# Optimization experiments

Measured on AMD Instinct MI355X. Metric: run time of the kernel, lower is better.

## Reference

```python
import jax, jax.numpy as jnp
import numpy as np


def _bilinear_sample(img, gx, gy):
    # img: [B,C,H,W]; gx,gy: [B,N] normalized coords in [-1,1]
    # Matches torch F.grid_sample(mode='bilinear', padding_mode='border', align_corners=False)
    B, C, H, W = img.shape
    ix = ((gx + 1.0) * W - 1.0) * 0.5
    iy = ((gy + 1.0) * H - 1.0) * 0.5
    ix = jnp.clip(ix, 0.0, W - 1.0)  # border padding: clip source coords
    iy = jnp.clip(iy, 0.0, H - 1.0)
    x0 = jnp.floor(ix); y0 = jnp.floor(iy)
    wx = ix - x0; wy = iy - y0
    x0i = x0.astype(jnp.int32); y0i = y0.astype(jnp.int32)
    x1i = jnp.minimum(x0i + 1, W - 1); y1i = jnp.minimum(y0i + 1, H - 1)
    imt = jnp.transpose(img, (0, 2, 3, 1))  # [B,H,W,C]
    b = jnp.arange(B)[:, None]
    v00 = imt[b, y0i, x0i]  # [B,N,C]
    v01 = imt[b, y0i, x1i]
    v10 = imt[b, y1i, x0i]
    v11 = imt[b, y1i, x1i]
    w00 = ((1 - wy) * (1 - wx))[..., None]
    w01 = ((1 - wy) * wx)[..., None]
    w10 = (wy * (1 - wx))[..., None]
    w11 = (wy * wx)[..., None]
    out = v00 * w00 + v01 * w01 + v10 * w10 + v11 * w11  # [B,N,C]
    return jnp.transpose(out, (0, 2, 1))  # [B,C,N]


def _conv1x1(W, b, x):
    # W: [Cout,Cin], b: [Cout], x: [B,Cin,N] -> [B,Cout,N]
    return jnp.einsum('oc,bcn->bon', W, x) + b[None, :, None]


def setup_inputs() -> dict:
    key = jax.random.key(0)
    ks = jax.random.split(key, 12)
    B, N = 4, 65536
    C_FEAT = 64
    CH = [67, 128, 128]
    x_loc = jax.random.uniform(ks[0], (B, 3, N), dtype=jnp.float32)
    x_feat = jax.random.normal(ks[1], (B, C_FEAT, N), dtype=jnp.float32)
    m0 = jax.random.normal(ks[2], (B, 64, 128, 128), dtype=jnp.float32)
    m1 = jax.random.normal(ks[3], (B, 128, 128, 128), dtype=jnp.float32)
    m2 = jax.random.normal(ks[4], (B, 256, 128, 128), dtype=jnp.float32)
    # SharedMLP params (kaiming-ish scale)
    W1 = jax.random.normal(ks[5], (CH[1], CH[0]), dtype=jnp.float32) * (1.0 / np.sqrt(CH[0]))
    b1 = jnp.zeros((CH[1],), dtype=jnp.float32)
    W2 = jax.random.normal(ks[6], (CH[2], CH[1]), dtype=jnp.float32) * (1.0 / np.sqrt(CH[1]))
    b2 = jnp.zeros((CH[2],), dtype=jnp.float32)
    # resid_loc: zero-init except identity on first two input channels (x/y of x_loc)
    Wr = jnp.zeros((2, CH[2] + 3), dtype=jnp.float32).at[0, 0].set(1.0).at[1, 1].set(1.0)
    br = jnp.zeros((2,), dtype=jnp.float32)
    return dict(x_loc=x_loc, x_feat=x_feat, m0=m0, m1=m1, m2=m2,
                W1=W1, b1=b1, W2=W2, b2=b2, Wr=Wr, br=br)


def reference(x_loc, x_feat, m0, m1, m2, W1, b1, W2, b2, Wr, br):
    # loc = Sequential(SharedMLP([67,128,128]), ReLU)
    h = jnp.concatenate([x_loc, x_feat], axis=1)          # [B,67,N]
    h = jax.nn.relu(_conv1x1(W1, b1, h))                  # [B,128,N]
    h = jax.nn.relu(_conv1x1(W2, b2, h))                  # [B,128,N]
    h = jnp.concatenate([x_loc, h], axis=1)               # [B,131,N]
    grid = _conv1x1(Wr, br, h)                            # [B,2,N]
    gx, gy = grid[:, 0, :], grid[:, 1, :]                 # grid last dim = (x, y)
    pooled = [_bilinear_sample(m, gx, gy) for m in (m0, m1, m2)]
    return jnp.concatenate(pooled, axis=1)                # [B,448,N]
```

## Files before the change

### kernel.cpp

```cpp
#include <hip/hip_runtime.h>
#include <hip/hip_bf16.h>

typedef __bf16 bf16x8 __attribute__((ext_vector_type(8)));
typedef __bf16 bf16x4 __attribute__((ext_vector_type(4)));
typedef float  f32x4  __attribute__((ext_vector_type(4)));

#define N_PTS  65536
#define B_SZ   4
#define P_TOT  (B_SZ * N_PTS)
#define PITCH1 104
#define PITCH2 136

__device__ __forceinline__ void gload_lds16(const float* g, float* l) {
    __builtin_amdgcn_global_load_lds(
        (const __attribute__((address_space(1))) void*)g,
        (__attribute__((address_space(3))) void*)l,
        16, 0, 0);
}

__global__ __launch_bounds__(256) void mlp_grid_kernel(
    const float* __restrict__ x_loc, const float* __restrict__ x_feat,
    const float* __restrict__ W1, const float* __restrict__ b1,
    const float* __restrict__ W2, const float* __restrict__ b2,
    const float* __restrict__ Wr, const float* __restrict__ br,
    float* __restrict__ grid_out)
{
    __shared__ __align__(16) union SmemU {
        __bf16 wbuf[128 * 128];
        struct {
            __bf16 stage[64 * PITCH1];
            __bf16 h1s[64 * PITCH2];
            float  gpart[16][2][64];
        } r;
    } u;

    const int tid = threadIdx.x;
    const int w   = tid >> 6;
    const int l   = tid & 63;
    const int q   = l >> 4;
    const int lp  = l & 15;

    for (int idx = tid; idx < 128 * 96; idx += 256) {
        const int o = idx / 96;
        const int k = idx - o * 96;
        u.wbuf[idx] = (__bf16)((k < 67) ? W1[o * 67 + k] : 0.0f);
    }
    __syncthreads();
    bf16x8 w1f[2][3];
    #pragma unroll
    for (int i = 0; i < 2; ++i) {
        const int o = (2 * w + i) * 16 + lp;
        #pragma unroll
        for (int ks = 0; ks < 3; ++ks)
            w1f[i][ks] = *(const bf16x8*)&u.wbuf[o * 96 + ks * 32 + q * 8];
    }
    __syncthreads();
    for (int idx = tid; idx < 128 * 128; idx += 256)
        u.wbuf[idx] = (__bf16)W2[idx];
    __syncthreads();
    bf16x8 w2f[2][4];
    #pragma unroll
    for (int i = 0; i < 2; ++i) {
        const int o = (2 * w + i) * 16 + lp;
        #pragma unroll
        for (int ks = 0; ks < 4; ++ks)
            w2f[i][ks] = *(const bf16x8*)&u.wbuf[o * 128 + ks * 32 + q * 8];
    }
    float b1v[2][4], b2v[2][4], wrp[2][2][4];
    #pragma unroll
    for (int i = 0; i < 2; ++i) {
        const int ob = (2 * w + i) * 16 + q * 4;
        #pragma unroll
        for (int r = 0; r < 4; ++r) {
            b1v[i][r]    = b1[ob + r];
            b2v[i][r]    = b2[ob + r];
            wrp[0][i][r] = Wr[0 * 131 + 3 + ob + r];
            wrp[1][i][r] = Wr[1 * 131 + 3 + ob + r];
        }
    }
    __syncthreads();

    for (int t = 0; t < 4; ++t) {
        const int pt0 = blockIdx.x * 256 + t * 64;

        {
            const int g4  = tid & 15;
            const int kk  = tid >> 4;
            const int ptg = g4 * 4;
            const int pp  = pt0 + ptg;
            const int bb  = pp >> 16;
            const int nn  = pp & 0xFFFF;
            for (int k = kk; k < 96; k += 16) {
                if (k < 67) {
                    const float4 v = (k < 3)
                        ? *(const float4*)&x_loc[((bb * 3 + k) << 16) | nn]
                        : *(const float4*)&x_feat[((bb * 64 + (k - 3)) << 16) | nn];
                    u.r.stage[(ptg + 0) * PITCH1 + k] = (__bf16)v.x;
                    u.r.stage[(ptg + 1) * PITCH1 + k] = (__bf16)v.y;
                    u.r.stage[(ptg + 2) * PITCH1 + k] = (__bf16)v.z;
                    u.r.stage[(ptg + 3) * PITCH1 + k] = (__bf16)v.w;
                } else if (k >= 67) {
                    u.r.stage[(ptg + 0) * PITCH1 + k] = (__bf16)0.0f;
                    u.r.stage[(ptg + 1) * PITCH1 + k] = (__bf16)0.0f;
                    u.r.stage[(ptg + 2) * PITCH1 + k] = (__bf16)0.0f;
                    u.r.stage[(ptg + 3) * PITCH1 + k] = (__bf16)0.0f;
                }
            }
        }
        __syncthreads();

        for (int col = 0; col < 4; ++col) {
            const int pt = col * 16 + lp;
            bf16x8 bfr[3];
            #pragma unroll
            for (int ks = 0; ks < 3; ++ks)
                bfr[ks] = *(const bf16x8*)&u.r.stage[pt * PITCH1 + ks * 32 + q * 8];
            #pragma unroll
            for (int i = 0; i < 2; ++i) {
                f32x4 acc = {0.f, 0.f, 0.f, 0.f};
                #pragma unroll
                for (int ks = 0; ks < 3; ++ks)
                    acc = __builtin_amdgcn_mfma_f32_16x16x32_bf16(w1f[i][ks], bfr[ks], acc, 0, 0, 0);
                bf16x4 hv;
                #pragma unroll
                for (int r = 0; r < 4; ++r)
                    hv[r] = (__bf16)fmaxf(acc[r] + b1v[i][r], 0.0f);
                *(bf16x4*)&u.r.h1s[pt * PITCH2 + (2 * w + i) * 16 + q * 4] = hv;
            }
        }
        __syncthreads();

        for (int col = 0; col < 4; ++col) {
            const int pt = col * 16 + lp;
            bf16x8 bfr[4];
            #pragma unroll
            for (int ks = 0; ks < 4; ++ks)
                bfr[ks] = *(const bf16x8*)&u.r.h1s[pt * PITCH2 + ks * 32 + q * 8];
            float p0 = 0.f, p1 = 0.f;
            #pragma unroll
            for (int i = 0; i < 2; ++i) {
                f32x4 acc = {0.f, 0.f, 0.f, 0.f};
                #pragma unroll
                for (int ks = 0; ks < 4; ++ks)
                    acc = __builtin_amdgcn_mfma_f32_16x16x32_bf16(w2f[i][ks], bfr[ks], acc, 0, 0, 0);
                #pragma unroll
                for (int r = 0; r < 4; ++r) {
                    const float v = fmaxf(acc[r] + b2v[i][r], 0.0f);
                    p0 += wrp[0][i][r] * v;
                    p1 += wrp[1][i][r] * v;
                }
            }
            u.r.gpart[w * 4 + q][0][pt] = p0;
            u.r.gpart[w * 4 + q][1][pt] = p1;
        }
        __syncthreads();

        if (tid < 128) {
            const int o  = tid >> 6;
            const int pt = tid & 63;
            const int pp = pt0 + pt;
            const int bb = pp >> 16;
            const int nn = pp & 0xFFFF;
            float s = br[o];
            #pragma unroll
            for (int c = 0; c < 3; ++c)
                s += Wr[o * 131 + c] * x_loc[((bb * 3 + c) << 16) | nn];
            #pragma unroll
            for (int g = 0; g < 16; ++g) s += u.r.gpart[g][o][pt];
            grid_out[o * P_TOT + pp] = s;
        }
    }
}

__global__ __launch_bounds__(1024) void sample_kernel(
    const float* __restrict__ m0, const float* __restrict__ m1,
    const float* __restrict__ m2, const float* __restrict__ grid,
    float* __restrict__ out)
{
    __shared__ float sbuf[2][128 * 128];
    __shared__ int redmn[16], redmx[16];

    const int tid  = threadIdx.x;
    const int wv   = tid >> 6;
    const int lane = tid & 63;
    const int p = blockIdx.x * 1024 + tid;
    const int b = p >> 16;
    const int n = p & 0xFFFF;
    const float gx = grid[p];
    const float gy = grid[P_TOT + p];

    float ix = ((gx + 1.0f) * 128.0f - 1.0f) * 0.5f;
    float iy = ((gy + 1.0f) * 128.0f - 1.0f) * 0.5f;
    ix = fminf(fmaxf(ix, 0.0f), 127.0f);
    iy = fminf(fmaxf(iy, 0.0f), 127.0f);
    const float x0f = floorf(ix);
    const float y0f = floorf(iy);
    const float wx = ix - x0f;
    const float wy = iy - y0f;
    const int x0 = (int)x0f, y0 = (int)y0f;
    const int x1 = min(x0 + 1, 127);
    const int y1 = min(y0 + 1, 127);
    const float w00 = (1.f - wy) * (1.f - wx);
    const float w01 = (1.f - wy) * wx;
    const float w10 = wy * (1.f - wx);
    const float w11 = wy * wx;

    int mn = y0, mx = y1;
    #pragma unroll
    for (int s = 32; s; s >>= 1) {
        mn = min(mn, __shfl_xor(mn, s));
        mx = max(mx, __shfl_xor(mx, s));
    }
    if (lane == 0) { redmn[wv] = mn; redmx[wv] = mx; }
    __syncthreads();
    #pragma unroll
    for (int i = 0; i < 16; ++i) { mn = min(mn, redmn[i]); mx = max(mx, redmx[i]); }

    int ymin = mn;
    int R = mx - mn + 1;
    if (R & 1) { if (ymin > 0) --ymin; ++R; }
    const int nchunk = R >> 1;

    const int a00 = (y0 - ymin) * 128 + x0;
    const int d01 = x1 - x0;
    const int d10 = (y1 - y0) * 128;

    auto slice = [&](int c) -> const float* {
        if (c < 64)  return m0 + ((size_t)(b * 64  + c)         << 14);
        if (c < 192) return m1 + ((size_t)(b * 128 + (c - 64))  << 14);
        return              m2 + ((size_t)(b * 256 + (c - 192)) << 14);
    };
    auto stage = [&](const float* src, int bsel) {
        const float* g = src + ymin * 128 + (lane << 2);
        for (int ch = wv; ch < nchunk; ch += 16)
            gload_lds16(g + (ch << 8), &sbuf[bsel][ch << 8]);
    };

    float* op = out + (size_t)(b * 448) * 65536 + n;

    stage(slice(0), 0);
    for (int c = 0; c < 448; ++c) {
        const int cur = c & 1;
        __syncthreads();
        if (c + 1 < 448) stage(slice(c + 1), cur ^ 1);
        const float* sb = sbuf[cur];
        const float v00 = sb[a00];
        const float v01 = sb[a00 + d01];
        const float v10 = sb[a00 + d10];
        const float v11 = sb[a00 + d01 + d10];
        const float v = w00 * v00 + w01 * v01 + w10 * v10 + w11 * v11;
        __builtin_nontemporal_store(v, op);
        op += 65536;
    }
}

extern "C" void kernel_launch(void* const* d_in, const int* in_sizes, int n_in,
                              void* d_out, int out_size, void* d_ws, size_t ws_size,
                              hipStream_t stream)
{
    (void)in_sizes; (void)n_in; (void)out_size; (void)ws_size;
    const float* x_loc  = (const float*)d_in[0];
    const float* x_feat = (const float*)d_in[1];
    const float* m0     = (const float*)d_in[2];
    const float* m1     = (const float*)d_in[3];
    const float* m2     = (const float*)d_in[4];
    const float* W1     = (const float*)d_in[5];
    const float* b1     = (const float*)d_in[6];
    const float* W2     = (const float*)d_in[7];
    const float* b2     = (const float*)d_in[8];
    const float* Wr     = (const float*)d_in[9];
    const float* br     = (const float*)d_in[10];
    float* out  = (float*)d_out;
    float* grid = (float*)d_ws;

    mlp_grid_kernel<<<dim3(P_TOT / 256), dim3(256), 0, stream>>>(
        x_loc, x_feat, W1, b1, W2, b2, Wr, br, grid);
    sample_kernel<<<dim3(P_TOT / 1024), dim3(1024), 0, stream>>>(
        m0, m1, m2, grid, out);
}
```

Before: 1.131 ms.

## Fuse MLP grid computation into sampler with bounding-box LDS staging

Merges the MLP grid kernel and the bilinear sampler into one 512-thread kernel that keeps grid coordinates in LDS instead of a workspace round-trip. Weights are pre-packed into MFMA fragment layout by a small one-block kernel. The sampler now stages only the x/y bounding box of each block's sample footprint (72-wide padded rows) with triple buffering and deferred stores, falling back to direct global gathers when the box is too large. This cuts LDS traffic per channel and raises occupancy, at the cost of an extra launch and a slow fallback path for scattered grids.

```diff
diff --git a/kernel.cpp b/kernel.cpp
--- a/kernel.cpp
+++ b/kernel.cpp
@@ -10,6 +10,11 @@
 #define P_TOT  (B_SZ * N_PTS)
 #define PITCH1 104
 #define PITCH2 136
+#define CPAD   72
+#define BUF_F  6144
+#define NCH    448
+#define WP1_ELEMS (8*3*64*8)
+#define WP2_ELEMS (8*4*64*8)
 
 __device__ __forceinline__ void gload_lds16(const float* g, float* l) {
     __builtin_amdgcn_global_load_lds(
@@ -18,92 +23,105 @@
         16, 0, 0);
 }
 
-__global__ __launch_bounds__(256) void mlp_grid_kernel(
+__global__ __launch_bounds__(256) void repack_weights(
+    const float* __restrict__ W1, const float* __restrict__ W2,
+    __bf16* __restrict__ wp)
+{
+    const int tid = threadIdx.x;
+    for (int idx = tid; idx < WP1_ELEMS; idx += 256) {
+        const int j8   = idx & 7;
+        const int l    = (idx >> 3) & 63;
+        const int rest = idx >> 9;
+        const int ks   = rest % 3;
+        const int j    = rest / 3;
+        const int row  = j * 16 + (l & 15);
+        const int k    = ks * 32 + ((l >> 4) << 3) + j8;
+        wp[idx] = (__bf16)((k < 67) ? W1[row * 67 + k] : 0.0f);
+    }
+    for (int idx = tid; idx < WP2_ELEMS; idx += 256) {
+        const int j8   = idx & 7;
+        const int l    = (idx >> 3) & 63;
+        const int rest = idx >> 9;
+        const int ks   = rest & 3;
+        const int j    = rest >> 2;
+        const int row  = j * 16 + (l & 15);
+        const int k    = ks * 32 + ((l >> 4) << 3) + j8;
+        wp[WP1_ELEMS + idx] = (__bf16)W2[row * 128 + k];
+    }
+}
+
+__global__ __launch_bounds__(512, 4) void fused_kernel(
     const float* __restrict__ x_loc, const float* __restrict__ x_feat,
-    const float* __restrict__ W1, const float* __restrict__ b1,
-    const float* __restrict__ W2, const float* __restrict__ b2,
+    const float* __restrict__ m0, const float* __restrict__ m1,
+    const float* __restrict__ m2,
+    const __bf16* __restrict__ wp,
+    const float* __restrict__ b1, const float* __restrict__ b2,
     const float* __restrict__ Wr, const float* __restrict__ br,
-    float* __restrict__ grid_out)
+    float* __restrict__ out)
 {
-    __shared__ __align__(16) union SmemU {
-        __bf16 wbuf[128 * 128];
+    __shared__ __align__(16) union Smem {
         struct {
             __bf16 stage[64 * PITCH1];
             __bf16 h1s[64 * PITCH2];
-            float  gpart[16][2][64];
-        } r;
+            float  gpart[8][2][64];
+            float  gxy[2][512];
+        } m;
+        float sbuf[3][BUF_F];
     } u;
+    __shared__ int redY0[8], redY1[8], redX0[8], redX1[8];
 
     const int tid = threadIdx.x;
     const int w   = tid >> 6;
     const int l   = tid & 63;
     const int q   = l >> 4;
     const int lp  = l & 15;
-
-    for (int idx = tid; idx < 128 * 96; idx += 256) {
-        const int o = idx / 96;
-        const int k = idx - o * 96;
-        u.wbuf[idx] = (__bf16)((k < 67) ? W1[o * 67 + k] : 0.0f);
-    }
-    __syncthreads();
-    bf16x8 w1f[2][3];
+    const int blk = blockIdx.x;
+    const int b   = blk >> 7;
+    const int n0  = (blk & 127) << 9;
+
+    bf16x8 w1f[3], w2f[4];
     #pragma unroll
-    for (int i = 0; i < 2; ++i) {
-        const int o = (2 * w + i) * 16 + lp;
-        #pragma unroll
-        for (int ks = 0; ks < 3; ++ks)
-            w1f[i][ks] = *(const bf16x8*)&u.wbuf[o * 96 + ks * 32 + q * 8];
-    }
-    __syncthreads();
-    for (int idx = tid; idx < 128 * 128; idx += 256)
-        u.wbuf[idx] = (__bf16)W2[idx];
-    __syncthreads();
-    bf16x8 w2f[2][4];
+    for (int ks = 0; ks < 3; ++ks)
+        w1f[ks] = *(const bf16x8*)&wp[((w * 3 + ks) * 64 + l) * 8];
     #pragma unroll
-    for (int i = 0; i < 2; ++i) {
-        const int o = (2 * w + i) * 16 + lp;
-        #pragma unroll
-        for (int ks = 0; ks < 4; ++ks)
-            w2f[i][ks] = *(const bf16x8*)&u.wbuf[o * 128 + ks * 32 + q * 8];
-    }
-    float b1v[2][4], b2v[2][4], wrp[2][2][4];
-    #pragma unroll
-    for (int i = 0; i < 2; ++i) {
-        const int ob = (2 * w + i) * 16 + q * 4;
+    for (int ks = 0; ks < 4; ++ks)
+        w2f[ks] = *(const bf16x8*)&wp[WP1_ELEMS + ((w * 4 + ks) * 64 + l) * 8];
+    float b1v[4], b2v[4], wrp0[4], wrp1[4];
+    {
+        const int ob = w * 16 + q * 4;
         #pragma unroll
         for (int r = 0; r < 4; ++r) {
-            b1v[i][r]    = b1[ob + r];
-            b2v[i][r]    = b2[ob + r];
-            wrp[0][i][r] = Wr[0 * 131 + 3 + ob + r];
-            wrp[1][i][r] = Wr[1 * 131 + 3 + ob + r];
-        }
-    }
-    __syncthreads();
-
-    for (int t = 0; t < 4; ++t) {
-        const int pt0 = blockIdx.x * 256 + t * 64;
+            b1v[r]  = b1[ob + r];
+            b2v[r]  = b2[ob + r];
+            wrp0[r] = Wr[0 * 131 + 3 + ob + r];
+            wrp1[r] = Wr[1 * 131 + 3 + ob + r];
+        }
+    }
+
+    for (int t = 0; t < 8; ++t) {
+        const int pt0n = n0 + t * 64;
 
         {
             const int g4  = tid & 15;
             const int kk  = tid >> 4;
             const int ptg = g4 * 4;
-            const int pp  = pt0 + ptg;
-            const int bb  = pp >> 16;
-            const int nn  = pp & 0xFFFF;
-            for (int k = kk; k < 96; k += 16) {
+            const int nn  = pt0n + ptg;
+            #pragma unroll
+            for (int kx = 0; kx < 3; ++kx) {
+                const int k = kk + kx * 32;
                 if (k < 67) {
                     const float4 v = (k < 3)
-                        ? *(const float4*)&x_loc[((bb * 3 + k) << 16) | nn]
-                        : *(const float4*)&x_feat[((bb * 64 + (k - 3)) << 16) | nn];
-                    u.r.stage[(ptg + 0) * PITCH1 + k] = (__bf16)v.x;
-                    u.r.stage[(ptg + 1) * PITCH1 + k] = (__bf16)v.y;
-                    u.r.stage[(ptg + 2) * PITCH1 + k] = (__bf16)v.z;
-                    u.r.stage[(ptg + 3) * PITCH1 + k] = (__bf16)v.w;
-                } else if (k >= 67) {
-                    u.r.stage[(ptg + 0) * PITCH1 + k] = (__bf16)0.0f;
-                    u.r.stage[(ptg + 1) * PITCH1 + k] = (__bf16)0.0f;
-                    u.r.stage[(ptg + 2) * PITCH1 + k] = (__bf16)0.0f;
-                    u.r.stage[(ptg + 3) * PITCH1 + k] = (__bf16)0.0f;
+                        ? *(const float4*)&x_loc[((b * 3 + k) << 16) | nn]
+                        : *(const float4*)&x_feat[((b * 64 + (k - 3)) << 16) | nn];
+                    u.m.stage[(ptg + 0) * PITCH1 + k] = (__bf16)v.x;
+                    u.m.stage[(ptg + 1) * PITCH1 + k] = (__bf16)v.y;
+                    u.m.stage[(ptg + 2) * PITCH1 + k] = (__bf16)v.z;
+                    u.m.stage[(ptg + 3) * PITCH1 + k] = (__bf16)v.w;
+                } else {
+                    u.m.stage[(ptg + 0) * PITCH1 + k] = (__bf16)0.0f;
+                    u.m.stage[(ptg + 1) * PITCH1 + k] = (__bf16)0.0f;
+                    u.m.stage[(ptg + 2) * PITCH1 + k] = (__bf16)0.0f;
+                    u.m.stage[(ptg + 3) * PITCH1 + k] = (__bf16)0.0f;
                 }
             }
         }
@@ -114,19 +132,16 @@
             bf16x8 bfr[3];
             #pragma unroll
             for (int ks = 0; ks < 3; ++ks)
-                bfr[ks] = *(const bf16x8*)&u.r.stage[pt * PITCH1 + ks * 32 + q * 8];
-            #pragma unroll
-            for (int i = 0; i < 2; ++i) {
-                f32x4 acc = {0.f, 0.f, 0.f, 0.f};
-                #pragma unroll
-                for (int ks = 0; ks < 3; ++ks)
-                    acc = __builtin_amdgcn_mfma_f32_16x16x32_bf16(w1f[i][ks], bfr[ks], acc, 0, 0, 0);
-                bf16x4 hv;
-                #pragma unroll
-                for (int r = 0; r < 4; ++r)
-                    hv[r] = (__bf16)fmaxf(acc[r] + b1v[i][r], 0.0f);
-                *(bf16x4*)&u.r.h1s[pt * PITCH2 + (2 * w + i) * 16 + q * 4] = hv;
-            }
+                bfr[ks] = *(const bf16x8*)&u.m.stage[pt * PITCH1 + ks * 32 + q * 8];
+            f32x4 acc = {0.f, 0.f, 0.f, 0.f};
+            #pragma unroll
+            for (int ks = 0; ks < 3; ++ks)
+                acc = __builtin_amdgcn_mfma_f32_16x16x32_bf16(w1f[ks], bfr[ks], acc, 0, 0, 0);
+            bf16x4 hv;
+            #pragma unroll
+            for (int r = 0; r < 4; ++r)
+                hv[r] = (__bf16)fmaxf(acc[r] + b1v[r], 0.0f);
+            *(bf16x4*)&u.m.h1s[pt * PITCH2 + w * 16 + q * 4] = hv;
         }
         __syncthreads();
 
@@ -135,59 +150,45 @@
             bf16x8 bfr[4];
             #pragma unroll
             for (int ks = 0; ks < 4; ++ks)
-                bfr[ks] = *(const bf16x8*)&u.r.h1s[pt * PITCH2 + ks * 32 + q * 8];
+                bfr[ks] = *(const bf16x8*)&u.m.h1s[pt * PITCH2 + ks * 32 + q * 8];
+            f32x4 acc = {0.f, 0.f, 0.f, 0.f};
+            #pragma unroll
+            for (int ks = 0; ks < 4; ++ks)
+                acc = __builtin_amdgcn_mfma_f32_16x16x32_bf16(w2f[ks], bfr[ks], acc, 0, 0, 0);
             float p0 = 0.f, p1 = 0.f;
             #pragma unroll
-            for (int i = 0; i < 2; ++i) {
-                f32x4 acc = {0.f, 0.f, 0.f, 0.f};
-                #pragma unroll
-                for (int ks = 0; ks < 4; ++ks)
-                    acc = __builtin_amdgcn_mfma_f32_16x16x32_bf16(w2f[i][ks], bfr[ks], acc, 0, 0, 0);
-                #pragma unroll
-                for (int r = 0; r < 4; ++r) {
-                    const float v = fmaxf(acc[r] + b2v[i][r], 0.0f);
-                    p0 += wrp[0][i][r] * v;
-                    p1 += wrp[1][i][r] * v;
-                }
+            for (int r = 0; r < 4; ++r) {
+                const float v = fmaxf(acc[r] + b2v[r], 0.0f);
+                p0 += wrp0[r] * v;
+                p1 += wrp1[r] * v;
             }
-            u.r.gpart[w * 4 + q][0][pt] = p0;
-            u.r.gpart[w * 4 + q][1][pt] = p1;
+            p0 += __shfl_xor(p0, 16); p0 += __shfl_xor(p0, 32);
+            p1 += __shfl_xor(p1, 16); p1 += __shfl_xor(p1, 32);
+            if (q == 0) {
+                u.m.gpart[w][0][pt] = p0;
+                u.m.gpart[w][1][pt] = p1;
+            }
         }
         __syncthreads();
 
         if (tid < 128) {
             const int o  = tid >> 6;
             const int pt = tid & 63;
-            const int pp = pt0 + pt;
-            const int bb = pp >> 16;
-            const int nn = pp & 0xFFFF;
+            const int nn = pt0n + pt;
             float s = br[o];
             #pragma unroll
             for (int c = 0; c < 3; ++c)
-                s += Wr[o * 131 + c] * x_loc[((bb * 3 + c) << 16) | nn];
-            #pragma unroll
-            for (int g = 0; g < 16; ++g) s += u.r.gpart[g][o][pt];
-            grid_out[o * P_TOT + pp] = s;
-        }
-    }
-}
-
-__global__ __launch_bounds__(1024) void sample_kernel(
-    const float* __restrict__ m0, const float* __restrict__ m1,
-    const float* __restrict__ m2, const float* __restrict__ grid,
-    float* __restrict__ out)
-{
-    __shared__ float sbuf[2][128 * 128];
-    __shared__ int redmn[16], redmx[16];
-
-    const int tid  = threadIdx.x;
-    const int wv   = tid >> 6;
-    const int lane = tid & 63;
-    const int p = blockIdx.x * 1024 + tid;
-    const int b = p >> 16;
-    const int n = p & 0xFFFF;
-    const float gx = grid[p];
-    const float gy = grid[P_TOT + p];
+                s += Wr[o * 131 + c] * x_loc[((b * 3 + c) << 16) | nn];
+            #pragma unroll
+            for (int g = 0; g < 8; ++g) s += u.m.gpart[g][o][pt];
+            u.m.gxy[o][t * 64 + pt] = s;
+        }
+    }
+    __syncthreads();
+
+    const float gx = u.m.gxy[0][tid];
+    const float gy = u.m.gxy[1][tid];
+    const int n = n0 + tid;
 
     float ix = ((gx + 1.0f) * 128.0f - 1.0f) * 0.5f;
     float iy = ((gy + 1.0f) * 128.0f - 1.0f) * 0.5f;
@@ -205,52 +206,89 @@
     const float w10 = wy * (1.f - wx);
     const float w11 = wy * wx;
 
-    int mn = y0, mx = y1;
+    int mnY = y0, mxY = y1, mnX = x0, mxX = x1;
     #pragma unroll
     for (int s = 32; s; s >>= 1) {
-        mn = min(mn, __shfl_xor(mn, s));
-        mx = max(mx, __shfl_xor(mx, s));
-    }
-    if (lane == 0) { redmn[wv] = mn; redmx[wv] = mx; }
+        mnY = min(mnY, __shfl_xor(mnY, s));
+        mxY = max(mxY, __shfl_xor(mxY, s));
+        mnX = min(mnX, __shfl_xor(mnX, s));
+        mxX = max(mxX, __shfl_xor(mxX, s));
+    }
+    if (l == 0) { redY0[w] = mnY; redY1[w] = mxY; redX0[w] = mnX; redX1[w] = mxX; }
     __syncthreads();
     #pragma unroll
-    for (int i = 0; i < 16; ++i) { mn = min(mn, redmn[i]); mx = max(mx, redmx[i]); }
-
-    int ymin = mn;
-    int R = mx - mn + 1;
-    if (R & 1) { if (ymin > 0) --ymin; ++R; }
-    const int nchunk = R >> 1;
-
-    const int a00 = (y0 - ymin) * 128 + x0;
-    const int d01 = x1 - x0;
-    const int d10 = (y1 - y0) * 128;
-
-    auto slice = [&](int c) -> const float* {
+    for (int i = 0; i < 8; ++i) {
+        mnY = min(mnY, redY0[i]); mxY = max(mxY, redY1[i]);
+        mnX = min(mnX, redX0[i]); mxX = max(mxX, redX1[i]);
+    }
+
+    const int ymin  = mnY;
+    const int R     = mxY - mnY + 1;
+    const int xminA = mnX & ~3;
+    const int width = mxX - xminA + 1;
+    const bool ok   = (width <= CPAD) && (R * CPAD <= BUF_F);
+
+    auto slice_ptr = [&](int c) -> const float* {
         if (c < 64)  return m0 + ((size_t)(b * 64  + c)         << 14);
         if (c < 192) return m1 + ((size_t)(b * 128 + (c - 64))  << 14);
         return              m2 + ((size_t)(b * 256 + (c - 192)) << 14);
     };
-    auto stage = [&](const float* src, int bsel) {
-        const float* g = src + ymin * 128 + (lane << 2);
-        for (int ch = wv; ch < nchunk; ch += 16)
-            gload_lds16(g + (ch << 8), &sbuf[bsel][ch << 8]);
-    };
-
-    float* op = out + (size_t)(b * 448) * 65536 + n;
-
-    stage(slice(0), 0);
-    for (int c = 0; c < 448; ++c) {
-        const int cur = c & 1;
-        __syncthreads();
-        if (c + 1 < 448) stage(slice(c + 1), cur ^ 1);
-        const float* sb = sbuf[cur];
-        const float v00 = sb[a00];
-        const float v01 = sb[a00 + d01];
-        const float v10 = sb[a00 + d10];
-        const float v11 = sb[a00 + d01 + d10];
-        const float v = w00 * v00 + w01 * v01 + w10 * v10 + w11 * v11;
-        __builtin_nontemporal_store(v, op);
-        op += 65536;
+
+    float* op = out + ((size_t)(b * 448) << 16) + n;
+
+    if (ok) {
+        const int nchunk = (R * CPAD + 255) >> 8;
+        const int a00 = (y0 - ymin) * CPAD + (x0 - xminA);
+        const int d01 = x1 - x0;
+        const int d10 = (y1 - y0) * CPAD;
+
+        auto stage = [&](int c, int bsel) {
+            const float* sp   = slice_ptr(c);
+            const float* src  = sp + ymin * 128 + xminA;
+            const float* gend = sp + 16384 - 4;
+            for (int ch = w; ch < nchunk; ch += 8) {
+                const int o   = (ch << 8) + (l << 2);
+                const int row = o / CPAD;
+                const int col = o - row * CPAD;
+                const float* g = src + row * 128 + col;
+                if (g > gend) g = gend;
+                gload_lds16(g, &u.sbuf[bsel][ch << 8]);
+            }
+        };
+
+        stage(0, 0);
+        stage(1, 1);
+        float vprev = 0.f;
+        float* opprev = op;
+        int cur = 0, nst = 2;
+        for (int c = 0; c < NCH; ++c) {
+            __syncthreads();
+            if (c) __builtin_nontemporal_store(vprev, opprev);
+            if (c + 2 < NCH) stage(c + 2, nst);
+            const float* sb = &u.sbuf[cur][0];
+            const float v00 = sb[a00];
+            const float v01 = sb[a00 + d01];
+            const float v10 = sb[a00 + d10];
+            const float v11 = sb[a00 + d01 + d10];
+            vprev  = w00 * v00 + w01 * v01 + w10 * v10 + w11 * v11;
+            opprev = op;
+            op += N_PTS;
+            cur = (cur == 2) ? 0 : cur + 1;
+            nst = (nst == 2) ? 0 : nst + 1;
+        }
+        __builtin_nontemporal_store(vprev, opprev);
+    } else {
+        const int o00 = y0 * 128 + x0;
+        const int o01 = y0 * 128 + x1;
+        const int o10 = y1 * 128 + x0;
+        const int o11 = y1 * 128 + x1;
+        for (int c = 0; c < NCH; ++c) {
+            const float* sp = slice_ptr(c);
+            const float v = w00 * sp[o00] + w01 * sp[o01]
+                          + w10 * sp[o10] + w11 * sp[o11];
+            __builtin_nontemporal_store(v, op);
+            op += N_PTS;
+        }
     }
 }
 
@@ -270,11 +308,10 @@
     const float* b2     = (const float*)d_in[8];
     const float* Wr     = (const float*)d_in[9];
     const float* br     = (const float*)d_in[10];
-    float* out  = (float*)d_out;
-    float* grid = (float*)d_ws;
-
-    mlp_grid_kernel<<<dim3(P_TOT / 256), dim3(256), 0, stream>>>(
-        x_loc, x_feat, W1, b1, W2, b2, Wr, br, grid);
-    sample_kernel<<<dim3(P_TOT / 1024), dim3(1024), 0, stream>>>(
-        m0, m1, m2, grid, out);
+    float*  out = (float*)d_out;
+    __bf16* wpk = (__bf16*)d_ws;
+
+    repack_weights<<<dim3(1), dim3(256), 0, stream>>>(W1, W2, wpk);
+    fused_kernel<<<dim3(P_TOT / 512), dim3(512), 0, stream>>>(
+        x_loc, x_feat, m0, m1, m2, wpk, b1, b2, Wr, br, out);
 }
```

New measurement: 1.077 ms. 4.8% less time.
